# Optimization experiments

Hardware: AMD Instinct MI355X
Metric: run time of the kernel (lower is better)

## Reference

```python
import jax, jax.numpy as jnp
import numpy as np

NEG = -1e30  # finite stand-in for -inf (safe under logsumexp)
EPS = 1e-7   # keras.backend.epsilon(): ctc_batch_cost does log(y_pred + eps)


def _ctc_loss(y_pred, y_true, input_length, label_length):
    # y_pred: [B,T,K] probabilities; blank index = K-1 (Keras convention)
    B, T, K = y_pred.shape
    L = y_true.shape[1]
    S = 2 * L + 1
    blank = K - 1
    log_probs = jnp.log(y_pred + EPS)  # [B,T,K]

    # extended label sequence: blank, l1, blank, l2, ..., blank  -> [B,S]
    ext = jnp.full((B, S), blank, dtype=y_true.dtype).at[:, 1::2].set(y_true)
    # skip transition (s-2 -> s) allowed iff s>=2, ext[s]!=blank, ext[s]!=ext[s-2]
    ext_sm2 = jnp.pad(ext[:, :-2], ((0, 0), (2, 0)), constant_values=blank)
    can_skip = (jnp.arange(S)[None, :] >= 2) & (ext != blank) & (ext != ext_sm2)

    in_len = input_length[:, 0]  # [B]

    # alpha_{-1}: probability 1 of being 'before' position 0
    alpha0 = jnp.full((B, S), NEG, dtype=log_probs.dtype).at[:, 0].set(0.0)

    lp_T = jnp.transpose(log_probs, (1, 0, 2))  # [T,B,K] for scan

    def step(carry, lp_t):
        alpha, t = carry
        lp = jnp.take_along_axis(lp_t, ext, axis=1)  # [B,S] emission logp
        a1 = jnp.pad(alpha[:, :-1], ((0, 0), (1, 0)), constant_values=NEG)
        a2 = jnp.pad(alpha[:, :-2], ((0, 0), (2, 0)), constant_values=NEG)
        a2 = jnp.where(can_skip, a2, NEG)
        new = lp + jax.nn.logsumexp(jnp.stack([alpha, a1, a2]), axis=0)
        active = (t < in_len)[:, None]  # freeze alpha past each sample's length
        return (jnp.where(active, new, alpha), t + 1), None

    (alpha, _), _ = jax.lax.scan(step, (alpha0, jnp.int32(0)), lp_T)

    # per-sample end positions: s = 2*label_len and s = 2*label_len - 1
    idx_last = 2 * label_length[:, 0]  # [B]
    end1 = jnp.take_along_axis(alpha, idx_last[:, None], axis=1)[:, 0]
    end2 = jnp.take_along_axis(alpha, jnp.maximum(idx_last - 1, 0)[:, None], axis=1)[:, 0]
    loss = -jnp.logaddexp(end1, end2)
    return loss[:, None]  # [B,1], matching ctc_batch_cost


def setup_inputs() -> dict:
    key = jax.random.key(0)
    k1, k2, k3, k4 = jax.random.split(key, 4)
    B, T, K, L = 512, 1024, 128, 64
    logits = jax.random.normal(k1, (B, T, K), dtype=jnp.float32)
    y_pred = jax.nn.softmax(logits, axis=-1)  # ctc_batch_cost expects probabilities
    y_true = jax.random.randint(k2, (B, L), 0, K - 1, dtype=jnp.int32)  # exclude blank
    input_length = jax.random.randint(k3, (B, 1), T // 2, T + 1, dtype=jnp.int32)
    label_length = jax.random.randint(k4, (B, 1), 8, L + 1, dtype=jnp.int32)
    return {"y_true": y_true, "y_pred": y_pred,
            "input_length": input_length, "label_length": label_length}


def reference(y_true, y_pred, input_length, label_length):
    return _ctc_loss(y_pred, y_true, input_length, label_length)
```

## Files before the change

### kernel.cpp

```cpp
#include <hip/hip_runtime.h>

#define EPSV (1e-7f)
#define LN2F (0.69314718055994531f)
#define NEGK (-(1 << 29))

constexpr int Tdim = 1024;
constexpr int Kdim = 128;
constexpr int Ldim = 64;
constexpr int BLK  = 32;
constexpr int WARM = 96;
constexpr int CENB = 175;

__device__ __forceinline__ void dma16(const float* g, float* l) {
    __builtin_amdgcn_global_load_lds(
        (const __attribute__((address_space(1))) unsigned int*)g,
        (__attribute__((address_space(3))) unsigned int*)l,
        16, 0, 0);
}

__device__ __forceinline__ float dpp_shr1_f(float x, float old) {
    return __int_as_float(__builtin_amdgcn_update_dpp(
        __float_as_int(old), __float_as_int(x), 0x138, 0xF, 0xF, false));
}
__device__ __forceinline__ int dpp_shr1_i(int x, int old) {
    return __builtin_amdgcn_update_dpp(old, x, 0x138, 0xF, 0xF, false);
}

__device__ __forceinline__ float hw_log2(float x) { return __builtin_amdgcn_logf(x); }
__device__ __forceinline__ int imax(int a, int b) { return a > b ? a : b; }

__global__ __launch_bounds__(64, 1) void ctc_fwd_kernel(
    const int* __restrict__ y_true,
    const float* __restrict__ y_pred,
    const int* __restrict__ in_len,
    const int* __restrict__ lab_len,
    float* __restrict__ out)
{
    const int b = blockIdx.x;
    const int lane = threadIdx.x;

    __shared__ float rows[2][BLK][Kdim];
    __shared__ float alpha_s[130];
    __shared__ int   ks_s[130];

    const float* yp  = y_pred + (size_t)b * Tdim * Kdim;
    const int lab = y_true[b * Ldim + lane];
    const int lab_prev = __shfl_up(lab, 1, 64);
    const bool skip = (lane > 0) && (lab != Kdim - 1) && (lab != lab_prev);
    const int steps = in_len[b];

    float a_e = (lane == 0) ? 1.0f : 0.0f;
    float a_o = 0.0f;
    float a_l = 0.0f;
    int   k_e = (lane == 0) ? 0 : NEGK;
    int   k_o = NEGK;
    int   k_l = NEGK;

    auto issue = [&](int t0, int buf) {
        #pragma unroll
        for (int u = 0; u < BLK / 2; ++u) {
            int t = t0 + 2 * u;
            t = (t > Tdim - 2) ? (Tdim - 2) : t;
            dma16(yp + (size_t)t * Kdim + 4 * lane, &rows[buf][2 * u][0]);
        }
    };

    auto step_slow = [&](float pl, float pb) {
        const float p_o = dpp_shr1_f(a_o, 0.0f);
        const int   pk  = dpp_shr1_i(k_o, NEGK);
        const int   pk3 = skip ? pk  : NEGK;
        const float p3v = skip ? p_o : 0.0f;
        const int kw1 = imax(k_e, pk);
        const float ne = pb * (ldexpf(a_e, k_e - kw1) + ldexpf(p_o, pk - kw1));
        const int kw2 = imax(imax(k_o, k_e), pk3);
        const float no = pl * (ldexpf(a_o, k_o - kw2) +
                               ldexpf(a_e, k_e - kw2) +
                               ldexpf(p3v, pk3 - kw2));
        const int kw3 = imax(k_l, k_o);
        const float nl = pb * (ldexpf(a_l, k_l - kw3) + ldexpf(a_o, k_o - kw3));
        a_e = ne; k_e = (ne == 0.0f) ? NEGK : kw1;
        a_o = no; k_o = (no == 0.0f) ? NEGK : kw2;
        a_l = nl; k_l = (nl == 0.0f) ? NEGK : kw3;
    };
    auto renorm1 = [](float& v, int& k) {
        const int mb = (__float_as_int(v) >> 23) & 0xff;
        if (mb != 0) { k += mb - 127; v *= __int_as_float((254 - mb) << 23); }
    };
    auto renorm_slow = [&]() { renorm1(a_e, k_e); renorm1(a_o, k_o); renorm1(a_l, k_l); };

    issue(0, 0);

    const int steps_full = steps & ~(BLK - 1);

    for (int tb = 0; tb < WARM; tb += BLK) {
        const int cur = (tb >> 5) & 1;
        asm volatile("s_waitcnt lgkmcnt(0)" ::: "memory");
        __builtin_amdgcn_sched_barrier(0);
        issue(tb + BLK, cur ^ 1);
        __builtin_amdgcn_sched_barrier(0);
        asm volatile("s_waitcnt vmcnt(16)" ::: "memory");
        __builtin_amdgcn_sched_barrier(0);
        float vl[BLK], vb[BLK];
        #pragma unroll
        for (int u = 0; u < BLK; ++u) {
            vl[u] = rows[cur][u][lab] + EPSV;
            vb[u] = rows[cur][u][Kdim - 1] + EPSV;
        }
        #pragma unroll
        for (int u = 0; u < BLK; ++u) {
            step_slow(vl[u], vb[u]);
            if ((u & 3) == 3) renorm_slow();
        }
    }

    int kk = imax(imax(k_e, k_o), k_l);
    a_e = ldexpf(a_e, k_e - kk + 48);
    a_o = ldexpf(a_o, k_o - kk + 48);
    a_l = ldexpf(a_l, k_l - kk + 48);
    kk -= 48;
    int d = dpp_shr1_i(kk, 0) - kk;

    auto renorm_fast = [&]() {
        const float m = fmaxf(fmaxf(a_e, a_o), a_l);
        const int mb = __float_as_int(m) >> 23;
        const float sc = __int_as_float((127 + CENB - mb) << 23);
        kk += mb - CENB;
        a_e *= sc; a_o *= sc; a_l *= sc;
        d = dpp_shr1_i(kk, 0) - kk;
    };
    auto step_fast = [&](float pl, float pb) {
        const float p_o  = dpp_shr1_f(a_o, 0.0f);
        const float p_a  = ldexpf(p_o, d);
        const float p_s  = skip ? p_a : 0.0f;
        const float ne = pb * (a_e + p_a);
        const float no = pl * (a_o + (a_e + p_s));
        const float nl = pb * (a_l + a_o);
        a_e = ne; a_o = no; a_l = nl;
    };

    for (int tb = WARM; tb < steps_full; tb += BLK) {
        const int cur = (tb >> 5) & 1;
        asm volatile("s_waitcnt lgkmcnt(0)" ::: "memory");
        __builtin_amdgcn_sched_barrier(0);
        issue(tb + BLK, cur ^ 1);
        __builtin_amdgcn_sched_barrier(0);
        asm volatile("s_waitcnt vmcnt(16)" ::: "memory");
        __builtin_amdgcn_sched_barrier(0);
        float vl[BLK], vb[BLK];
        #pragma unroll
        for (int u = 0; u < BLK; ++u) {
            vl[u] = rows[cur][u][lab] + EPSV;
            vb[u] = rows[cur][u][Kdim - 1] + EPSV;
        }
        #pragma unroll
        for (int u = 0; u < BLK; ++u) {
            if ((u & 3) == 0) renorm_fast();
            step_fast(vl[u], vb[u]);
        }
    }

    {
        const int cur = (steps_full >> 5) & 1;
        asm volatile("s_waitcnt vmcnt(0)" ::: "memory");
        __builtin_amdgcn_sched_barrier(0);
        float vl[BLK], vb[BLK];
        #pragma unroll
        for (int u = 0; u < BLK; ++u) {
            vl[u] = rows[cur][u][lab] + EPSV;
            vb[u] = rows[cur][u][Kdim - 1] + EPSV;
        }
        #pragma unroll
        for (int u = 0; u < BLK; ++u) {
            if (steps_full + u < steps) {
                if ((u & 3) == 0) renorm_fast();
                step_fast(vl[u], vb[u]);
            }
        }
    }

    alpha_s[2 * lane]     = a_e;
    alpha_s[2 * lane + 1] = a_o;
    ks_s[2 * lane]        = kk;
    ks_s[2 * lane + 1]    = kk;
    if (lane == 63) { alpha_s[128] = a_l; ks_s[128] = kk; }
    __syncthreads();

    if (lane == 0) {
        const int ll = lab_len[b];
        const int i1 = 2 * ll;
        const int i2 = i1 - 1;
        const float v1 = alpha_s[i1], v2 = alpha_s[i2];
        const int   k1 = ks_s[i1],   k2 = ks_s[i2];
        const int   K  = imax(k1, k2);
        const float s  = ldexpf(v1, k1 - K) + ldexpf(v2, k2 - K);
        out[b] = -LN2F * (hw_log2(s) + (float)K);
    }
}

extern "C" void kernel_launch(void* const* d_in, const int* in_sizes, int n_in,
                              void* d_out, int out_size, void* d_ws, size_t ws_size,
                              hipStream_t stream) {
    const int*   y_true   = (const int*)d_in[0];
    const float* y_pred   = (const float*)d_in[1];
    const int*   in_len   = (const int*)d_in[2];
    const int*   lab_len  = (const int*)d_in[3];
    float* out = (float*)d_out;

    const int B = in_sizes[0] / Ldim;
    ctc_fwd_kernel<<<B, 64, 0, stream>>>(y_true, y_pred, in_len, lab_len, out);
}
```

Baseline: 67.54 us.

## Fuse two CTC recurrence steps into one algebraic double-step update

Replaces two sequential single-step alpha updates in the main loop with a closed-form two-step update. It precomputes emission products and uses DPP shifts by one and two lanes with per-lane exponent offsets (d, d2). The aim is to shorten the serial dependency chain through cross-lane shifts, which is the latency-bound critical path. In exchange each step does more arithmetic and needs an extra skip mask from the neighbouring lane, and the renormalisation interval in real steps is unchanged.

```diff
diff --git a/kernel.cpp b/kernel.cpp
--- a/kernel.cpp
+++ b/kernel.cpp
@@ -46,7 +46,8 @@
     const float* yp  = y_pred + (size_t)b * Tdim * Kdim;
     const int lab = y_true[b * Ldim + lane];
     const int lab_prev = __shfl_up(lab, 1, 64);
-    const bool skip = (lane > 0) && (lab != Kdim - 1) && (lab != lab_prev);
+    const bool skip  = (lane > 0) && (lab != Kdim - 1) && (lab != lab_prev);
+    const bool skipm = (lane > 0) && __shfl_up((int)skip, 1, 64);
     const int steps = in_len[b];
 
     float a_e = (lane == 0) ? 1.0f : 0.0f;
@@ -118,7 +119,7 @@
     a_o = ldexpf(a_o, k_o - kk + 48);
     a_l = ldexpf(a_l, k_l - kk + 48);
     kk -= 48;
-    int d = dpp_shr1_i(kk, 0) - kk;
+    int d = 0, d2 = 0;
 
     auto renorm_fast = [&]() {
         const float m = fmaxf(fmaxf(a_e, a_o), a_l);
@@ -126,8 +127,12 @@
         const float sc = __int_as_float((127 + CENB - mb) << 23);
         kk += mb - CENB;
         a_e *= sc; a_o *= sc; a_l *= sc;
-        d = dpp_shr1_i(kk, 0) - kk;
-    };
+        const int kkm  = dpp_shr1_i(kk, 0);
+        const int kkmm = dpp_shr1_i(kkm, 0);
+        d  = kkm  - kk;
+        d2 = kkmm - kk;
+    };
+
     auto step_fast = [&](float pl, float pb) {
         const float p_o  = dpp_shr1_f(a_o, 0.0f);
         const float p_a  = ldexpf(p_o, d);
@@ -138,6 +143,34 @@
         a_e = ne; a_o = no; a_l = nl;
     };
 
+    auto step2 = [&](float pl1, float pb1, float pl2, float pb2) {
+        const float pl1m = dpp_shr1_f(pl1, 0.0f);
+        const float pb12 = pb1 * pb2;
+        const float A  = pb2 * pl1m;
+        const float B  = pl2 * pl1;
+        const float C  = pl2 * pb1;
+        const float F  = pb2 * pl1;
+        const float cD0 = skip ? (pl2 * pl1m) : 0.0f;
+        const float k1 = pb12 + A;
+        const float k2 = B + C;
+        const float k3 = C + cD0;
+        const float k4 = pb12 + F;
+        const float Om  = dpp_shr1_f(a_o, 0.0f);
+        const float Em  = dpp_shr1_f(a_e, 0.0f);
+        const float Omm = dpp_shr1_f(Om, 0.0f);
+        const float z   = ldexpf(Om, d);
+        const float ze  = ldexpf(Em, d);
+        const float zz  = ldexpf(Omm, d2);
+        const float zs  = skip  ? z  : 0.0f;
+        const float zzc = skipm ? zz : 0.0f;
+        const float t1  = ze + zzc;
+        const float ne = fmaf(pb12, a_e, fmaf(k1, z, A * t1));
+        const float no = fmaf(B, a_o, fmaf(k2, a_e,
+                         fmaf(k3, z, fmaf(B, zs, cD0 * t1))));
+        const float nl = fmaf(pb12, a_l, fmaf(k4, a_o, fmaf(F, a_e, F * zs)));
+        a_e = ne; a_o = no; a_l = nl;
+    };
+
     for (int tb = WARM; tb < steps_full; tb += BLK) {
         const int cur = (tb >> 5) & 1;
         asm volatile("s_waitcnt lgkmcnt(0)" ::: "memory");
@@ -153,9 +186,9 @@
             vb[u] = rows[cur][u][Kdim - 1] + EPSV;
         }
         #pragma unroll
-        for (int u = 0; u < BLK; ++u) {
-            if ((u & 3) == 0) renorm_fast();
-            step_fast(vl[u], vb[u]);
+        for (int f = 0; f < BLK / 2; ++f) {
+            if ((f & 1) == 0) renorm_fast();
+            step2(vl[2 * f], vb[2 * f], vl[2 * f + 1], vb[2 * f + 1]);
         }
     }
 
```

After: 75.58 us. +11.9%, slower.
